# Kernel tuning notes

Hardware: AMD Instinct MI355X
Metric: run time of the kernel (lower is better)

The kernel has to match this reference:

```python
import jax, jax.numpy as jnp
import numpy as np

B, T, D, N, H = 2, 2048, 2048, 16, 128
WINDOW = 1024
SOFT_CAP = 50.0
K_MASK = -2.3819763e+38
MAX_WAVELENGTH = 10000


def apply_rope(x, positions, head_dim):
    # x: [B, T, N, H], positions: [B, T]
    fraction = 2.0 * jnp.arange(head_dim // 2, dtype=jnp.float32) / head_dim
    timescale = MAX_WAVELENGTH ** fraction                      # [H/2]
    sinusoid = positions[..., None].astype(jnp.float32) / timescale  # [B, T, H/2]
    sinusoid = sinusoid[..., None, :]                           # [B, T, 1, H/2]
    sin, cos = jnp.sin(sinusoid), jnp.cos(sinusoid)
    first, second = jnp.split(x, 2, axis=-1)
    out = jnp.concatenate([first * cos - second * sin,
                           second * cos + first * sin], axis=-1)
    return out.astype(x.dtype)


def setup_inputs() -> dict:
    key = jax.random.key(0)
    k1, k2, k3 = jax.random.split(key, 3)
    x = jax.random.normal(k1, (B, T, D), dtype=jnp.float32)
    w_qkv = jax.random.normal(k2, (3, N, D, H), dtype=jnp.float32) * (D ** -0.5)
    w_out = jax.random.normal(k3, (N, H, D), dtype=jnp.float32) * ((N * H) ** -0.5)
    segment_pos = jnp.broadcast_to(jnp.arange(T, dtype=jnp.int32), (B, T))
    # causal attention mask [B, T, S]
    causal = jnp.tril(jnp.ones((T, T), dtype=jnp.bool_))
    attn_mask = jnp.broadcast_to(causal, (B, T, T))
    return {"x": x, "w_qkv": w_qkv, "w_out": w_out,
            "segment_pos": segment_pos, "attn_mask": attn_mask}


def reference(x, w_qkv, w_out, segment_pos, attn_mask):
    # QKV projection: [3, B, T, N, H]
    q, k, v = jnp.einsum('BTD,SNDH->SBTNH', x, w_qkv)
    q = apply_rope(q, segment_pos, H) * (H ** -0.5)
    k = apply_rope(k, segment_pos, H)
    logits = jnp.einsum('BTNH,BSNH->BTNS', q, k)
    # soft cap
    logits = jnp.tanh(logits / SOFT_CAP) * SOFT_CAP
    # sliding-window mask combined with causal mask
    ones = jnp.ones_like(attn_mask)
    sliding = jnp.triu(ones, -WINDOW + 1) & jnp.tril(ones, WINDOW - 1)
    mask = sliding & attn_mask                                   # [B, T, S]
    padded = jnp.where(mask[:, :, None, :], logits, K_MASK)
    probs = jax.nn.softmax(padded, axis=-1).astype(k.dtype)
    encoded = jnp.einsum('BTNS,BSNH->BTNH', probs, v)
    return jnp.einsum('BTNH,NHD->BTD', encoded, w_out)
```

## Files before the change

kernel.cpp:

```cpp
#include <hip/hip_runtime.h>

#define B_ 2
#define T_ 2048
#define D_ 2048
#define N_ 16
#define H_ 128
constexpr int WIN = 1024;

typedef __attribute__((ext_vector_type(8))) short s16x8;
typedef __attribute__((ext_vector_type(4))) float f32x4;
typedef __attribute__((ext_vector_type(4))) unsigned short u16x4;

typedef const __attribute__((address_space(1))) void cglobal_void;
typedef __attribute__((address_space(3))) void lds_void;

__device__ __forceinline__ unsigned short f2b(float f) {
  union { float f; unsigned u; } v; v.f = f;
  unsigned r = v.u + 0x7FFFu + ((v.u >> 16) & 1u);
  return (unsigned short)(r >> 16);
}
__device__ __forceinline__ float b2f(unsigned short u) {
  union { unsigned u; float f; } v; v.u = ((unsigned)u) << 16;
  return v.f;
}

__global__ __launch_bounds__(256) void detect_kernel(
    const unsigned short* __restrict__ x, int* __restrict__ flag) {
  __shared__ int cnt[256];
  const int tid = threadIdx.x;
  int c = 0;
  for (int i = tid; i < 4096; i += 256) {
    const unsigned short u = x[2 * i];
    const int e = (u >> 7) & 0xFF;
    if (e >= 154) ++c;
  }
  cnt[tid] = c;
  __syncthreads();
  for (int s = 128; s > 0; s >>= 1) {
    if (tid < s) cnt[tid] += cnt[tid + s];
    __syncthreads();
  }
  if (tid == 0) *flag = cnt[0];
}

__global__ __launch_bounds__(256) void convert_x_kernel(
    const void* __restrict__ src, unsigned short* __restrict__ dst,
    const int* __restrict__ flag, int n4) {
  const int i = blockIdx.x * 256 + threadIdx.x;
  if (i >= n4) return;
  const bool isf = (*flag > 64);
  u16x4 o;
  if (isf) {
    const float4 f = ((const float4*)src)[i];
    o[0] = f2b(f.x); o[1] = f2b(f.y); o[2] = f2b(f.z); o[3] = f2b(f.w);
  } else {
    o = ((const u16x4*)src)[i];
  }
  *(u16x4*)(dst + 4 * (size_t)i) = o;
}

__global__ __launch_bounds__(256) void transpose_kernel(
    const void* __restrict__ src, unsigned short* __restrict__ dst,
    int R, int C, const int* __restrict__ flag) {
  __shared__ unsigned short tile[32][33];
  const bool isf = (*flag > 64);
  const int c0 = blockIdx.x * 32, r0 = blockIdx.y * 32;
  const size_t base = (size_t)blockIdx.z * R * C;
  const int tx = threadIdx.x, ty = threadIdx.y;
#pragma unroll
  for (int j = 0; j < 32; j += 8) {
    const size_t idx = base + (size_t)(r0 + ty + j) * C + c0 + tx;
    tile[ty + j][tx] = isf ? f2b(((const float*)src)[idx])
                           : ((const unsigned short*)src)[idx];
  }
  __syncthreads();
#pragma unroll
  for (int j = 0; j < 32; j += 8)
    dst[base + (size_t)(c0 + ty + j) * R + r0 + tx] = tile[tx][ty + j];
}

__global__ __launch_bounds__(256) void transpose_bf16_kernel(
    const unsigned short* __restrict__ src, unsigned short* __restrict__ dst,
    int R, int C) {
  __shared__ unsigned short tile[32][33];
  const int c0 = blockIdx.x * 32, r0 = blockIdx.y * 32;
  const size_t base = (size_t)blockIdx.z * R * C;
  const int tx = threadIdx.x, ty = threadIdx.y;
#pragma unroll
  for (int j = 0; j < 32; j += 8)
    tile[ty + j][tx] = src[base + (size_t)(r0 + ty + j) * C + c0 + tx];
  __syncthreads();
#pragma unroll
  for (int j = 0; j < 32; j += 8)
    dst[base + (size_t)(c0 + ty + j) * R + r0 + tx] = tile[tx][ty + j];
}

__global__ __launch_bounds__(256) void gemm128_kernel(
    const unsigned short* __restrict__ A,
    const unsigned short* __restrict__ Bt,
    void* __restrict__ outp,
    int mode, const int* __restrict__ flag) {
  constexpr int K = D_;
  __shared__ unsigned short As[128 * 64];
  __shared__ unsigned short Bs[128 * 64];
  const int tid = threadIdx.x;
  const int lane = tid & 63;
  const int lr = lane & 15, lq = lane >> 4;
  const int wave = tid >> 6;
  const int wm = (wave >> 1) * 64, wn = (wave & 1) * 64;
  const size_t m0 = (size_t)blockIdx.x * 128;
  const unsigned short* pA = A + m0 * K;
  const unsigned short* pB = Bt + (size_t)blockIdx.y * 128 * K;

  f32x4 acc[4][4] = {};

  const int cg = (tid & 7) ^ ((tid >> 3) & 7);
  size_t goff[4];
#pragma unroll
  for (int j = 0; j < 4; ++j)
    goff[j] = (size_t)(j * 32 + (tid >> 3)) * K + cg * 8;

  for (int k0 = 0; k0 < K; k0 += 64) {
    __syncthreads();
#pragma unroll
    for (int j = 0; j < 4; ++j) {
      __builtin_amdgcn_global_load_lds((cglobal_void*)(pA + goff[j] + k0),
                                       (lds_void*)(As + (size_t)(j * 256 + tid) * 8), 16, 0, 0);
      __builtin_amdgcn_global_load_lds((cglobal_void*)(pB + goff[j] + k0),
                                       (lds_void*)(Bs + (size_t)(j * 256 + tid) * 8), 16, 0, 0);
    }
    __syncthreads();
#pragma unroll
    for (int kq = 0; kq < 2; ++kq) {
      const int co = (((kq << 2) + lq) ^ (lr & 7)) * 8;
      s16x8 af[4], bfr[4];
#pragma unroll
      for (int mb = 0; mb < 4; ++mb)
        af[mb] = *(const s16x8*)(As + (wm + mb * 16 + lr) * 64 + co);
#pragma unroll
      for (int nb = 0; nb < 4; ++nb)
        bfr[nb] = *(const s16x8*)(Bs + (wn + nb * 16 + lr) * 64 + co);
#pragma unroll
      for (int mb = 0; mb < 4; ++mb)
#pragma unroll
        for (int nb = 0; nb < 4; ++nb)
          acc[mb][nb] = __builtin_amdgcn_mfma_f32_16x16x32_bf16(af[mb], bfr[nb], acc[mb][nb], 0, 0, 0);
    }
  }

  if (mode == 0) {
    const bool isf = (*flag > 64);
#pragma unroll
    for (int mb = 0; mb < 4; ++mb) {
      const size_t r = m0 + wm + mb * 16 + lq * 4;
#pragma unroll
      for (int nb = 0; nb < 4; ++nb) {
        const size_t c = (size_t)blockIdx.y * 128 + wn + nb * 16 + lr;
#pragma unroll
        for (int i = 0; i < 4; ++i) {
          if (isf) ((float*)outp)[(r + i) * D_ + c] = acc[mb][nb][i];
          else ((unsigned short*)outp)[(r + i) * D_ + c] = f2b(acc[mb][nb][i]);
        }
      }
    }
  } else {
    unsigned short* op = (unsigned short*)outp;
    const int s = blockIdx.y >> 4, n = blockIdx.y & 15;
    const size_t SB = (size_t)B_ * N_ * T_ * H_;
#pragma unroll
    for (int mb = 0; mb < 4; ++mb) {
#pragma unroll
      for (int i = 0; i < 4; ++i) {
        const size_t r = m0 + wm + mb * 16 + lq * 4 + i;
        const int b = (int)(r >> 11);
        const int t = (int)(r & 2047);
        const size_t base = s * SB + (size_t)(b * N_ + n) * T_ * H_ + (size_t)t * H_;
#pragma unroll
        for (int nb = 0; nb < 4; ++nb)
          op[base + wn + nb * 16 + lr] = f2b(acc[mb][nb][i]);
      }
    }
  }
}

__global__ __launch_bounds__(256) void rope_kernel(unsigned short* __restrict__ qk) {
  const int tid = threadIdx.x;
  const int lane = tid & 63;
  const size_t row = (size_t)blockIdx.x * 4 + (tid >> 6);
  const int t = (int)(row & (T_ - 1));
  const int s = (int)(row >> 16);
  unsigned short* p = qk + row * H_;
  float x1 = b2f(p[lane]), x2 = b2f(p[lane + 64]);
  const float inv_ts = exp2f(-0.20762050f * (float)lane);
  float sv, cv;
  __sincosf((float)t * inv_ts, &sv, &cv);
  float o1 = x1 * cv - x2 * sv;
  float o2 = x2 * cv + x1 * sv;
  if (s == 0) { o1 *= 0.08838834764831845f; o2 *= 0.08838834764831845f; }
  p[lane] = f2b(o1);
  p[lane + 64] = f2b(o2);
}

__global__ __launch_bounds__(256, 4) void attn_kernel(
    const unsigned short* __restrict__ qkv,
    const unsigned short* __restrict__ vt,
    unsigned short* __restrict__ enc) {
  const int tid = threadIdx.x, lane = tid & 63, wave = tid >> 6;
  const int lr = lane & 15, lq = lane >> 4;
  const int bn = blockIdx.x;
  const int b = bn >> 4, n = bn & 15;
  const int t0 = blockIdx.y * 64;
  const size_t SB = (size_t)B_ * N_ * T_ * H_;
  const unsigned short* qp = qkv + (size_t)bn * T_ * H_;
  const unsigned short* kp = qp + SB;
  const unsigned short* vp = vt + (size_t)bn * T_ * H_;

  __shared__ unsigned short Ks[64 * 128];
  __shared__ unsigned short Vt[128 * 64];
  unsigned short* Ps = Ks + wave * 1024;

  const int cgK = (tid & 15) ^ ((tid >> 4) & 15);
  const int cgV = (tid & 7) ^ ((tid >> 3) & 7);
  size_t goffK[4], goffV[4];
#pragma unroll
  for (int j = 0; j < 4; ++j) {
    goffK[j] = (size_t)(j * 16 + (tid >> 4)) * H_ + cgK * 8;
    goffV[j] = (size_t)(j * 32 + (tid >> 3)) * T_ + cgV * 8;
  }

  s16x8 aq[4];
  {
    const int t = t0 + wave * 16 + lr;
#pragma unroll
    for (int kc = 0; kc < 4; ++kc)
      aq[kc] = *(const s16x8*)(qp + (size_t)t * H_ + kc * 32 + lq * 8);
  }

  f32x4 oacc[8] = {};
  float lp[4] = {0.f, 0.f, 0.f, 0.f};

  const int s_lo = (t0 >= WIN - 1) ? ((t0 - (WIN - 1)) & ~63) : 0;
  constexpr float C_IN = 0.05770780f;
  constexpr float M_SCALE = -144.269504f;
  constexpr float M_BIAS = 86.56f;

  for (int s0 = s_lo; s0 <= t0 + 63; s0 += 64) {
    __syncthreads();
#pragma unroll
    for (int j = 0; j < 4; ++j) {
      __builtin_amdgcn_global_load_lds((cglobal_void*)(kp + (size_t)s0 * H_ + goffK[j]),
                                       (lds_void*)(Ks + (size_t)(j * 256 + tid) * 8), 16, 0, 0);
      __builtin_amdgcn_global_load_lds((cglobal_void*)(vp + goffV[j] + s0),
                                       (lds_void*)(Vt + (size_t)(j * 256 + tid) * 8), 16, 0, 0);
    }
    __syncthreads();

    float p[4][4];
#pragma unroll
    for (int sb = 0; sb < 4; ++sb) {
      f32x4 a = {};
#pragma unroll
      for (int kc = 0; kc < 4; ++kc) {
        const int co = (((kc << 2) + lq) ^ lr) * 8;
        s16x8 bk = *(const s16x8*)(Ks + (sb * 16 + lr) * 128 + co);
        a = __builtin_amdgcn_mfma_f32_16x16x32_bf16(aq[kc], bk, a, 0, 0, 0);
      }
#pragma unroll
      for (int i = 0; i < 4; ++i) {
        const float u = exp2f(a[i] * C_IN);
        const float r = __builtin_amdgcn_rcpf(u + 1.0f);
        p[sb][i] = exp2f(fmaf(r, M_SCALE, M_BIAS));
      }
    }

    const bool interior = (s0 + 63 <= t0) && (s0 >= t0 + 63 - (WIN - 1));
    if (!interior) {
#pragma unroll
      for (int sb = 0; sb < 4; ++sb) {
        const int key = s0 + sb * 16 + lr;
#pragma unroll
        for (int i = 0; i < 4; ++i) {
          const int t = t0 + wave * 16 + lq * 4 + i;
          if (key > t || key < t - (WIN - 1)) p[sb][i] = 0.0f;
        }
      }
    }
#pragma unroll
    for (int sb = 0; sb < 4; ++sb)
#pragma unroll
      for (int i = 0; i < 4; ++i) lp[i] += p[sb][i];

    __syncthreads();
#pragma unroll
    for (int sb = 0; sb < 4; ++sb)
#pragma unroll
      for (int i = 0; i < 4; ++i) {
        const int row = lq * 4 + i;
        const int cph = ((sb * 2 + (lr >> 3)) ^ (row & 7));
        Ps[row * 64 + cph * 8 + (lr & 7)] = f2b(p[sb][i]);
      }
    __syncthreads();

    s16x8 ap[2];
#pragma unroll
    for (int kc = 0; kc < 2; ++kc)
      ap[kc] = *(const s16x8*)(Ps + lr * 64 + ((((kc << 2) + lq) ^ (lr & 7)) * 8));

#pragma unroll
    for (int hb = 0; hb < 8; ++hb) {
#pragma unroll
      for (int kc = 0; kc < 2; ++kc) {
        const int co = (((kc << 2) + lq) ^ (lr & 7)) * 8;
        s16x8 bv = *(const s16x8*)(Vt + (hb * 16 + lr) * 64 + co);
        oacc[hb] = __builtin_amdgcn_mfma_f32_16x16x32_bf16(ap[kc], bv, oacc[hb], 0, 0, 0);
      }
    }
  }

#pragma unroll
  for (int i = 0; i < 4; ++i) {
#pragma unroll
    for (int off = 1; off < 16; off <<= 1)
      lp[i] += __shfl_xor(lp[i], off, 64);
  }

#pragma unroll
  for (int i = 0; i < 4; ++i) {
    const int t = t0 + wave * 16 + lq * 4 + i;
    const float inv = 1.0f / lp[i];
    const size_t rowb = ((size_t)b * T_ + t) * (N_ * H_) + (size_t)n * H_;
#pragma unroll
    for (int hb = 0; hb < 8; ++hb)
      enc[rowb + hb * 16 + lr] = f2b(oacc[hb][i] * inv);
  }
}

extern "C" void kernel_launch(void* const* d_in, const int* in_sizes, int n_in,
                              void* d_out, int out_size, void* d_ws, size_t ws_size,
                              hipStream_t stream) {
  const void* x     = d_in[0];
  const void* w_qkv = d_in[1];
  const void* w_out = d_in[2];

  char* wsb = (char*)d_ws;
  int* flag = (int*)wsb;
  const size_t MB = 1048576;
  unsigned short* xc    = (unsigned short*)(wsb + 64);
  unsigned short* wqkvT = (unsigned short*)(wsb + 64 + 16 * MB);
  unsigned short* qkv   = (unsigned short*)(wsb + 64 + 40 * MB);
  unsigned short* vt    = xc;
  unsigned short* enc   = wqkvT;
  unsigned short* woutT = (unsigned short*)(wsb + 64 + 32 * MB);
  unsigned short* v     = qkv + 2 * (size_t)B_ * N_ * T_ * H_;

  detect_kernel<<<1, 256, 0, stream>>>((const unsigned short*)x, flag);
  convert_x_kernel<<<8192, 256, 0, stream>>>(x, xc, flag, B_ * T_ * D_ / 4);
  transpose_kernel<<<dim3(4, 64, 48), dim3(32, 8), 0, stream>>>(w_qkv, wqkvT, 2048, 128, flag);
  gemm128_kernel<<<dim3(32, 48), 256, 0, stream>>>(xc, wqkvT, qkv, 1, flag);
  rope_kernel<<<32768, 256, 0, stream>>>(qkv);
  transpose_bf16_kernel<<<dim3(4, 64, 32), dim3(32, 8), 0, stream>>>(v, vt, 2048, 128);
  transpose_kernel<<<dim3(64, 64, 1), dim3(32, 8), 0, stream>>>(w_out, woutT, 2048, 2048, flag);
  attn_kernel<<<dim3(32, 32), 256, 0, stream>>>(qkv, vt, enc);
  gemm128_kernel<<<dim3(32, 16), 256, 0, stream>>>(enc, woutT, d_out, 0, flag);
}
```

Baseline: 459.0 us.

## Double attention query tile to 128 rows and fuse Q RoPE into attention

Each attention block now handles 128 query rows (32 per wave, two MFMA row-blocks), so every K/V tile loaded into LDS serves twice as many queries and the grid halves. RoPE and scaling for Q move into the attention kernel's Q-fragment load, so the standalone rope kernel only processes K and its launch shrinks. The costs are doubled accumulator registers (launch bounds lowered from 4 to 2 blocks per CU), more masked work per block near the window edges, and bf16 rounding of Q now happening after rotation inside the kernel.

After: 459.8 us. No clear change (+0.2%).

```diff
diff --git a/kernel.cpp b/kernel.cpp
--- a/kernel.cpp
+++ b/kernel.cpp
@@ -183,25 +183,21 @@
   }
 }
 
-__global__ __launch_bounds__(256) void rope_kernel(unsigned short* __restrict__ qk) {
+__global__ __launch_bounds__(256) void rope_kernel(unsigned short* __restrict__ k) {
   const int tid = threadIdx.x;
   const int lane = tid & 63;
   const size_t row = (size_t)blockIdx.x * 4 + (tid >> 6);
   const int t = (int)(row & (T_ - 1));
-  const int s = (int)(row >> 16);
-  unsigned short* p = qk + row * H_;
+  unsigned short* p = k + row * H_;
   float x1 = b2f(p[lane]), x2 = b2f(p[lane + 64]);
   const float inv_ts = exp2f(-0.20762050f * (float)lane);
   float sv, cv;
   __sincosf((float)t * inv_ts, &sv, &cv);
-  float o1 = x1 * cv - x2 * sv;
-  float o2 = x2 * cv + x1 * sv;
-  if (s == 0) { o1 *= 0.08838834764831845f; o2 *= 0.08838834764831845f; }
-  p[lane] = f2b(o1);
-  p[lane + 64] = f2b(o2);
-}
-
-__global__ __launch_bounds__(256, 4) void attn_kernel(
+  p[lane] = f2b(x1 * cv - x2 * sv);
+  p[lane + 64] = f2b(x2 * cv + x1 * sv);
+}
+
+__global__ __launch_bounds__(256, 2) void attn_kernel(
     const unsigned short* __restrict__ qkv,
     const unsigned short* __restrict__ vt,
     unsigned short* __restrict__ enc) {
@@ -209,7 +205,7 @@
   const int lr = lane & 15, lq = lane >> 4;
   const int bn = blockIdx.x;
   const int b = bn >> 4, n = bn & 15;
-  const int t0 = blockIdx.y * 64;
+  const int t0 = blockIdx.y * 128;
   const size_t SB = (size_t)B_ * N_ * T_ * H_;
   const unsigned short* qp = qkv + (size_t)bn * T_ * H_;
   const unsigned short* kp = qp + SB;
@@ -217,7 +213,7 @@
 
   __shared__ unsigned short Ks[64 * 128];
   __shared__ unsigned short Vt[128 * 64];
-  unsigned short* Ps = Ks + wave * 1024;
+  unsigned short* Ps = Ks + wave * 2048;
 
   const int cgK = (tid & 15) ^ ((tid >> 4) & 15);
   const int cgV = (tid & 7) ^ ((tid >> 3) & 7);
@@ -228,23 +224,38 @@
     goffV[j] = (size_t)(j * 32 + (tid >> 3)) * T_ + cgV * 8;
   }
 
-  s16x8 aq[4];
-  {
-    const int t = t0 + wave * 16 + lr;
+  s16x8 aq[2][4];
+#pragma unroll
+  for (int mb = 0; mb < 2; ++mb) {
+    const int t = t0 + wave * 32 + mb * 16 + lr;
 #pragma unroll
     for (int kc = 0; kc < 4; ++kc)
-      aq[kc] = *(const s16x8*)(qp + (size_t)t * H_ + kc * 32 + lq * 8);
-  }
-
-  f32x4 oacc[8] = {};
-  float lp[4] = {0.f, 0.f, 0.f, 0.f};
-
-  const int s_lo = (t0 >= WIN - 1) ? ((t0 - (WIN - 1)) & ~63) : 0;
+      aq[mb][kc] = *(const s16x8*)(qp + (size_t)t * H_ + kc * 32 + lq * 8);
+#pragma unroll
+    for (int kc = 0; kc < 2; ++kc) {
+#pragma unroll
+      for (int j = 0; j < 8; ++j) {
+        const int i = kc * 32 + lq * 8 + j;
+        const float inv_ts = exp2f(-0.20762050f * (float)i);
+        float sv, cv;
+        __sincosf((float)t * inv_ts, &sv, &cv);
+        const float x1 = b2f((unsigned short)aq[mb][kc][j]);
+        const float x2 = b2f((unsigned short)aq[mb][kc + 2][j]);
+        aq[mb][kc][j] = (short)f2b((x1 * cv - x2 * sv) * 0.08838834764831845f);
+        aq[mb][kc + 2][j] = (short)f2b((x2 * cv + x1 * sv) * 0.08838834764831845f);
+      }
+    }
+  }
+
+  f32x4 oacc[2][8] = {};
+  float lp[2][4] = {};
+
+  const int s_lo = (t0 >= 1024) ? (t0 - 1024) : 0;
   constexpr float C_IN = 0.05770780f;
   constexpr float M_SCALE = -144.269504f;
   constexpr float M_BIAS = 86.56f;
 
-  for (int s0 = s_lo; s0 <= t0 + 63; s0 += 64) {
+  for (int s0 = s_lo; s0 <= t0 + 127; s0 += 64) {
     __syncthreads();
 #pragma unroll
     for (int j = 0; j < 4; ++j) {
@@ -255,56 +266,69 @@
     }
     __syncthreads();
 
-    float p[4][4];
+    float p[2][4][4];
 #pragma unroll
     for (int sb = 0; sb < 4; ++sb) {
-      f32x4 a = {};
+      f32x4 a[2] = {};
 #pragma unroll
       for (int kc = 0; kc < 4; ++kc) {
         const int co = (((kc << 2) + lq) ^ lr) * 8;
         s16x8 bk = *(const s16x8*)(Ks + (sb * 16 + lr) * 128 + co);
-        a = __builtin_amdgcn_mfma_f32_16x16x32_bf16(aq[kc], bk, a, 0, 0, 0);
-      }
-#pragma unroll
-      for (int i = 0; i < 4; ++i) {
-        const float u = exp2f(a[i] * C_IN);
-        const float r = __builtin_amdgcn_rcpf(u + 1.0f);
-        p[sb][i] = exp2f(fmaf(r, M_SCALE, M_BIAS));
-      }
-    }
-
-    const bool interior = (s0 + 63 <= t0) && (s0 >= t0 + 63 - (WIN - 1));
+#pragma unroll
+        for (int mb = 0; mb < 2; ++mb)
+          a[mb] = __builtin_amdgcn_mfma_f32_16x16x32_bf16(aq[mb][kc], bk, a[mb], 0, 0, 0);
+      }
+#pragma unroll
+      for (int mb = 0; mb < 2; ++mb)
+#pragma unroll
+        for (int i = 0; i < 4; ++i) {
+          const float u = exp2f(a[mb][i] * C_IN);
+          const float r = __builtin_amdgcn_rcpf(u + 1.0f);
+          p[mb][sb][i] = exp2f(fmaf(r, M_SCALE, M_BIAS));
+        }
+    }
+
+    const bool interior = (s0 + 63 <= t0) && (s0 >= t0 + 127 - (WIN - 1));
     if (!interior) {
 #pragma unroll
       for (int sb = 0; sb < 4; ++sb) {
         const int key = s0 + sb * 16 + lr;
 #pragma unroll
+        for (int mb = 0; mb < 2; ++mb)
+#pragma unroll
+          for (int i = 0; i < 4; ++i) {
+            const int t = t0 + wave * 32 + mb * 16 + lq * 4 + i;
+            if (key > t || key < t - (WIN - 1)) p[mb][sb][i] = 0.0f;
+          }
+      }
+    }
+#pragma unroll
+    for (int mb = 0; mb < 2; ++mb)
+#pragma unroll
+      for (int sb = 0; sb < 4; ++sb)
+#pragma unroll
+        for (int i = 0; i < 4; ++i) lp[mb][i] += p[mb][sb][i];
+
+    __syncthreads();
+#pragma unroll
+    for (int mb = 0; mb < 2; ++mb)
+#pragma unroll
+      for (int sb = 0; sb < 4; ++sb)
+#pragma unroll
         for (int i = 0; i < 4; ++i) {
-          const int t = t0 + wave * 16 + lq * 4 + i;
-          if (key > t || key < t - (WIN - 1)) p[sb][i] = 0.0f;
+          const int row = mb * 16 + lq * 4 + i;
+          const int cph = ((sb * 2 + (lr >> 3)) ^ (row & 7));
+          Ps[row * 64 + cph * 8 + (lr & 7)] = f2b(p[mb][sb][i]);
         }
-      }
-    }
-#pragma unroll
-    for (int sb = 0; sb < 4; ++sb)
-#pragma unroll
-      for (int i = 0; i < 4; ++i) lp[i] += p[sb][i];
-
-    __syncthreads();
-#pragma unroll
-    for (int sb = 0; sb < 4; ++sb)
-#pragma unroll
-      for (int i = 0; i < 4; ++i) {
-        const int row = lq * 4 + i;
-        const int cph = ((sb * 2 + (lr >> 3)) ^ (row & 7));
-        Ps[row * 64 + cph * 8 + (lr & 7)] = f2b(p[sb][i]);
-      }
-    __syncthreads();
-
-    s16x8 ap[2];
-#pragma unroll
-    for (int kc = 0; kc < 2; ++kc)
-      ap[kc] = *(const s16x8*)(Ps + lr * 64 + ((((kc << 2) + lq) ^ (lr & 7)) * 8));
+    __syncthreads();
+
+    s16x8 ap[2][2];
+#pragma unroll
+    for (int mb = 0; mb < 2; ++mb)
+#pragma unroll
+      for (int kc = 0; kc < 2; ++kc)
+        ap[mb][kc] = *(const s16x8*)(Ps + (mb * 16 + lr) * 64 +
+                                     ((((kc << 2) + lq) ^ (lr & 7)) * 8));
 
 #pragma unroll
     for (int hb = 0; hb < 8; ++hb) {
@@ -312,27 +336,33 @@
       for (int kc = 0; kc < 2; ++kc) {
         const int co = (((kc << 2) + lq) ^ (lr & 7)) * 8;
         s16x8 bv = *(const s16x8*)(Vt + (hb * 16 + lr) * 64 + co);
-        oacc[hb] = __builtin_amdgcn_mfma_f32_16x16x32_bf16(ap[kc], bv, oacc[hb], 0, 0, 0);
-      }
-    }
-  }
-
-#pragma unroll
-  for (int i = 0; i < 4; ++i) {
-#pragma unroll
-    for (int off = 1; off < 16; off <<= 1)
-      lp[i] += __shfl_xor(lp[i], off, 64);
-  }
-
-#pragma unroll
-  for (int i = 0; i < 4; ++i) {
-    const int t = t0 + wave * 16 + lq * 4 + i;
-    const float inv = 1.0f / lp[i];
-    const size_t rowb = ((size_t)b * T_ + t) * (N_ * H_) + (size_t)n * H_;
-#pragma unroll
-    for (int hb = 0; hb < 8; ++hb)
-      enc[rowb + hb * 16 + lr] = f2b(oacc[hb][i] * inv);
-  }
+#pragma unroll
+        for (int mb = 0; mb < 2; ++mb)
+          oacc[mb][hb] = __builtin_amdgcn_mfma_f32_16x16x32_bf16(ap[mb][kc], bv, oacc[mb][hb], 0, 0, 0);
+      }
+    }
+  }
+
+#pragma unroll
+  for (int mb = 0; mb < 2; ++mb)
+#pragma unroll
+    for (int i = 0; i < 4; ++i) {
+#pragma unroll
+      for (int off = 1; off < 16; off <<= 1)
+        lp[mb][i] += __shfl_xor(lp[mb][i], off, 64);
+    }
+
+#pragma unroll
+  for (int mb = 0; mb < 2; ++mb)
+#pragma unroll
+    for (int i = 0; i < 4; ++i) {
+      const int t = t0 + wave * 32 + mb * 16 + lq * 4 + i;
+      const float inv = 1.0f / lp[mb][i];
+      const size_t rowb = ((size_t)b * T_ + t) * (N_ * H_) + (size_t)n * H_;
+#pragma unroll
+      for (int hb = 0; hb < 8; ++hb)
+        enc[rowb + hb * 16 + lr] = f2b(oacc[mb][hb][i] * inv);
+    }
 }
 
 extern "C" void kernel_launch(void* const* d_in, const int* in_sizes, int n_in,
@@ -351,15 +381,16 @@
   unsigned short* vt    = xc;
   unsigned short* enc   = wqkvT;
   unsigned short* woutT = (unsigned short*)(wsb + 64 + 32 * MB);
+  unsigned short* k     = qkv + (size_t)B_ * N_ * T_ * H_;
   unsigned short* v     = qkv + 2 * (size_t)B_ * N_ * T_ * H_;
 
   detect_kernel<<<1, 256, 0, stream>>>((const unsigned short*)x, flag);
   convert_x_kernel<<<8192, 256, 0, stream>>>(x, xc, flag, B_ * T_ * D_ / 4);
   transpose_kernel<<<dim3(4, 64, 48), dim3(32, 8), 0, stream>>>(w_qkv, wqkvT, 2048, 128, flag);
   gemm128_kernel<<<dim3(32, 48), 256, 0, stream>>>(xc, wqkvT, qkv, 1, flag);
-  rope_kernel<<<32768, 256, 0, stream>>>(qkv);
+  rope_kernel<<<16384, 256, 0, stream>>>(k);
   transpose_bf16_kernel<<<dim3(4, 64, 32), dim3(32, 8), 0, stream>>>(v, vt, 2048, 128);
   transpose_kernel<<<dim3(64, 64, 1), dim3(32, 8), 0, stream>>>(w_out, woutT, 2048, 2048, flag);
-  attn_kernel<<<dim3(32, 32), 256, 0, stream>>>(qkv, vt, enc);
+  attn_kernel<<<dim3(32, 16), 256, 0, stream>>>(qkv, vt, enc);
   gemm128_kernel<<<dim3(32, 16), 256, 0, stream>>>(enc, woutT, d_out, 0, flag);
 }
```
